# Optimization experiments

Hardware: AMD Instinct MI355X
Metric: run time of the kernel (lower is better)

Reference implementation:

```python
import jax, jax.numpy as jnp
import numpy as np
from jax import lax

HEADS = 8  # ensembles * cells

def _conv(x, w, padding, groups):
    # NCHW grouped 2D convolution, stride 1
    return lax.conv_general_dilated(
        x, w, window_strides=(1, 1), padding=padding,
        feature_group_count=groups,
        dimension_numbers=('NCHW', 'OIHW', 'NCHW'))


def setup_inputs() -> dict:
    key = jax.random.key(0)
    ks = jax.random.split(key, 16)
    N, Cin, H, W = 8, 128, 36, 36
    C = 256                      # out_channels
    hc = C // HEADS              # head_channels = 32
    s = jnp.float32(0.05)        # weight scale to keep logits sane
    f32 = jnp.float32
    inp = {
        'x':  jax.random.normal(ks[0], (N, Cin, H, W), f32),
        'h0': jnp.zeros((N, C, H, W), f32),
        'c0': jnp.zeros((N, C, H, W), f32),
        'Wx': jax.random.normal(ks[1], (C, Cin, 1, 1), f32) * s,
        'Wq': jax.random.normal(ks[2], (C, 2 * hc, 3, 3), f32) * s,
        'Wk': jax.random.normal(ks[3], (C, 2 * hc, 3, 3), f32) * s,
        'Wv': jax.random.normal(ks[4], (C, 2 * hc, 3, 3), f32) * s,
        'Wi1': jax.random.normal(ks[5], (C, hc, 1, 1), f32) * s,
        'Wi2': jax.random.normal(ks[6], (C, 2 * hc, 3, 3), f32) * s,
        'bi': jnp.zeros((C,), f32),
        'Wf1': jax.random.normal(ks[7], (C, hc, 1, 1), f32) * s,
        'Wf2': jax.random.normal(ks[8], (C, 2 * hc, 3, 3), f32) * s,
        'bf': jnp.zeros((C,), f32),
        'Wg1': jax.random.normal(ks[9], (C, hc, 1, 1), f32) * s,
        'Wg2': jax.random.normal(ks[10], (C, 2 * hc, 3, 3), f32) * s,
        'bg': jnp.zeros((C,), f32),
        'Wo1': jax.random.normal(ks[11], (C, hc, 1, 1), f32) * s,
        'Wo2': jax.random.normal(ks[12], (C, 2 * hc, 3, 3), f32) * s,
        'bo': jnp.zeros((C,), f32),
        'tau': jnp.full((HEADS,), hc ** (-0.5), f32),
    }
    return inp


def reference(x, h0, c0, Wx, Wq, Wk, Wv, Wi1, Wi2, bi,
              Wf1, Wf2, bf, Wg1, Wg2, bg, Wo1, Wo2, bo, tau):
    N, _, H, W = x.shape
    G = tau.shape[0]
    # input projection (1x1 conv, no groups, no bias)
    xx = _conv(x, Wx, 'VALID', 1)          # [N, C, H, W]
    C = xx.shape[1]
    hc = C // G
    # stack x and h per head: [N, G, 2, hc, H, W] -> [N, 2C, H, W]
    xh = jnp.stack([xx.reshape(N, G, hc, H, W),
                    h0.reshape(N, G, hc, H, W)], axis=2)
    xh = xh.reshape(N, 2 * C, H, W)
    # q padded (SAME), k/v unpadded (VALID) -> mismatched spatial extents
    q = _conv(xh, Wq, 'SAME', G).reshape(N, G, hc, H * W)          # Q = H*W
    kc = _conv(xh, Wk, 'VALID', G)
    Dh, Dw = kc.shape[2], kc.shape[3]
    k = kc.reshape(N, G, hc, Dh * Dw)                              # D = (H-ks+1)*(W-ks+1)
    v = _conv(xh, Wv, 'VALID', G).reshape(N, G, hc, Dh * Dw)
    # attention: tau-scaled channel contraction, softmax over key positions
    logits = jnp.einsum('g,ngcq,ngcd->ngqd', tau, q, k)            # [N,G,Q,D]
    attn = jax.nn.softmax(logits, axis=3)
    a = jnp.einsum('ngcd,ngqd->ngcq', v, attn).reshape(N, C, H, W)

    def gate(W1, W2, b):
        # grouped 1x1 conv on a + grouped kxk SAME conv on xh + bias
        return (_conv(a, W1, 'VALID', G) + _conv(xh, W2, 'SAME', G)
                + b[None, :, None, None])

    i = jax.nn.sigmoid(gate(Wi1, Wi2, bi))
    f = jax.nn.sigmoid(gate(Wf1, Wf2, bf))
    g = jnp.tanh(gate(Wg1, Wg2, bg))
    o = jax.nn.sigmoid(gate(Wo1, Wo2, bo))
    c = f * c0 + i * g
    h = o * jnp.tanh(c)
    return h
```

## Files before the change

### kernel.cpp

```cpp
#include <hip/hip_runtime.h>
#include <math.h>

#define NN  8
#define CIN 128
#define HW  1296
#define CC  256
#define DDS 1156

typedef __attribute__((ext_vector_type(8))) short bvec8;
typedef __attribute__((ext_vector_type(4))) float fvec4;

__device__ __forceinline__ float sigmoidf_(float x) {
    return 1.f / (1.f + __expf(-x));
}
__device__ __forceinline__ float tanhf_(float x) {
    float xa = fminf(fmaxf(x, -15.f), 15.f);
    float e = __expf(2.f * xa);
    return (e - 1.f) / (e + 1.f);
}
__device__ __forceinline__ unsigned short f2bf(float f) {
    unsigned int u = __float_as_uint(f);
    u = (u + 0x7FFFu + ((u >> 16) & 1u)) >> 16;
    return (unsigned short)u;
}
__device__ __forceinline__ unsigned int cvtpk_bf16(float a, float b) {
    unsigned int r;
    asm("v_cvt_pk_bf16_f32 %0, %1, %2" : "=v"(r) : "v"(a), "v"(b));
    return r;
}

__global__ void k_prep(const float* __restrict__ x, const float* __restrict__ h0,
                       const float* __restrict__ Wx,
                       const float* __restrict__ Wq, const float* __restrict__ Wk,
                       const float* __restrict__ Wv, const float* __restrict__ tau,
                       const float* __restrict__ Wi2, const float* __restrict__ Wf2,
                       const float* __restrict__ Wg2, const float* __restrict__ Wo2,
                       const float* __restrict__ Wi1, const float* __restrict__ Wf1,
                       const float* __restrict__ Wg1, const float* __restrict__ Wo1,
                       unsigned short* __restrict__ xb, unsigned short* __restrict__ h0b,
                       unsigned short* __restrict__ apx, unsigned short* __restrict__ apq,
                       unsigned short* __restrict__ apg2, unsigned short* __restrict__ apg1) {
    int t = blockIdx.x * 256 + threadIdx.x;
    union { unsigned short us[8]; bvec8 v; } pk;
    if (t < 165888) {
        int p = t % 1296; int t2 = t / 1296;
        int icb = t2 % 16, n = t2 / 16;
        #pragma unroll
        for (int j = 0; j < 8; ++j)
            pk.us[j] = f2bf(x[(size_t)(n * CIN + icb * 8 + j) * HW + p]);
        *(bvec8*)(xb + (size_t)t * 8) = pk.v;
    } else if (t < 497664) {
        int u = t - 165888;
        int p = u % 1296; int t2 = u / 1296;
        int ocb = t2 % 32, n = t2 / 32;
        #pragma unroll
        for (int j = 0; j < 8; ++j)
            pk.us[j] = f2bf(h0[(size_t)(n * CC + ocb * 8 + j) * HW + p]);
        *(bvec8*)(h0b + (size_t)u * 8) = pk.v;
    } else if (t < 552960) {
        int u = t - 497664;
        int lane = u & 63;
        int t2 = u >> 6;
        int mf = t2 % 6, t3 = t2 / 6;
        int s = t3 % 18, g = t3 / 18;
        int kyx = s >> 1, icb = s & 1;
        int ky = kyx / 3, kx = kyx % 3;
        int m = mf * 16 + (lane & 15);
        int conv = m >> 5, cl = m & 31, co = g * 32 + cl;
        int ic0 = icb * 32 + (lane >> 4) * 8;
        const float* W = (conv == 0) ? Wq : (conv == 1 ? Wk : Wv);
        float scale = (conv == 0) ? tau[g] : 1.f;
        #pragma unroll
        for (int j = 0; j < 8; ++j)
            pk.us[j] = f2bf(W[((co * 64 + ic0 + j) * 3 + ky) * 3 + kx] * scale);
        *(bvec8*)(apq + (size_t)u * 8) = pk.v;
    } else if (t < 557056) {
        int u = t - 552960;
        int lane = u & 63;
        int t2 = u >> 6;
        int mf = t2 % 16, s = t2 / 16;
        int co = mf * 16 + (lane & 15);
        int k0 = s * 32 + (lane >> 4) * 8;
        #pragma unroll
        for (int j = 0; j < 8; ++j)
            pk.us[j] = f2bf(Wx[co * CIN + k0 + j]);
        *(bvec8*)(apx + (size_t)u * 8) = pk.v;
    } else if (t < 630784) {
        int u = t - 557056;
        int lane = u & 63;
        int t2 = u >> 6;
        int mf = t2 % 8, t3 = t2 / 8;
        int s = t3 % 18, g = t3 / 18;
        int kyx = s >> 1, icb = s & 1;
        int ky = kyx / 3, kx = kyx % 3;
        int m = mf * 16 + (lane & 15);
        int gate = m >> 5, cl = m & 31, co = g * 32 + cl;
        int ic0 = icb * 32 + (lane >> 4) * 8;
        const float* W = (gate == 0) ? Wi2 : (gate == 1 ? Wf2 : (gate == 2 ? Wg2 : Wo2));
        #pragma unroll
        for (int j = 0; j < 8; ++j)
            pk.us[j] = f2bf(W[((co * 64 + ic0 + j) * 3 + ky) * 3 + kx]);
        *(bvec8*)(apg2 + (size_t)u * 8) = pk.v;
    } else if (t < 634880) {
        int u = t - 630784;
        int lane = u & 63;
        int t2 = u >> 6;
        int mf = t2 % 8, g = t2 / 8;
        int m = mf * 16 + (lane & 15);
        int gate = m >> 5, cl = m & 31, co = g * 32 + cl;
        int k0 = (lane >> 4) * 8;
        const float* W = (gate == 0) ? Wi1 : (gate == 1 ? Wf1 : (gate == 2 ? Wg1 : Wo1));
        #pragma unroll
        for (int j = 0; j < 8; ++j)
            pk.us[j] = f2bf(W[co * 32 + k0 + j]);
        *(bvec8*)(apg1 + (size_t)u * 8) = pk.v;
    }
}

__global__ __launch_bounds__(256) void k_xx_mfma(
        const unsigned short* __restrict__ xb, const unsigned short* __restrict__ apx,
        unsigned short* __restrict__ xxb) {
    int bid = blockIdx.x;
    int n = bid / 27, pc = bid % 27;
    int tid = threadIdx.x;
    int w = tid >> 6, lane = tid & 63;
    int ln = lane & 15, kgrp = lane >> 4;
    const bvec8* A = (const bvec8*)apx;
    bvec8 af[4][4];
    #pragma unroll
    for (int s = 0; s < 4; ++s)
        #pragma unroll
        for (int i = 0; i < 4; ++i)
            af[s][i] = A[(s * 16 + w * 4 + i) * 64 + lane];
    fvec4 acc[4][3];
    #pragma unroll
    for (int i = 0; i < 4; ++i)
        #pragma unroll
        for (int jn = 0; jn < 3; ++jn)
            acc[i][jn] = fvec4{0.f, 0.f, 0.f, 0.f};
    #pragma unroll
    for (int s = 0; s < 4; ++s) {
        #pragma unroll
        for (int jn = 0; jn < 3; ++jn) {
            int p = pc * 48 + jn * 16 + ln;
            bvec8 bfr = *(const bvec8*)(xb + ((size_t)(n * 16 + s * 4 + kgrp) * HW + p) * 8);
            #pragma unroll
            for (int i = 0; i < 4; ++i)
                acc[i][jn] = __builtin_amdgcn_mfma_f32_16x16x32_bf16(af[s][i], bfr, acc[i][jn], 0, 0, 0);
        }
    }
    #pragma unroll
    for (int i = 0; i < 4; ++i) {
        int co0 = (w * 4 + i) * 16 + kgrp * 4;
        int icb = co0 >> 3, sub = co0 & 7;
        #pragma unroll
        for (int jn = 0; jn < 3; ++jn) {
            int p = pc * 48 + jn * 16 + ln;
            union { unsigned short us[4]; unsigned long long u; } pk;
            #pragma unroll
            for (int r = 0; r < 4; ++r) pk.us[r] = f2bf(acc[i][jn][r]);
            *(unsigned long long*)(xxb + ((size_t)(n * 32 + icb) * HW + p) * 8 + sub) = pk.u;
        }
    }
}

__global__ __launch_bounds__(384) void k_qkv_mfma(
        const unsigned short* __restrict__ xxb, const unsigned short* __restrict__ h0b,
        const unsigned short* __restrict__ apq,
        unsigned short* __restrict__ qT, unsigned short* __restrict__ kT,
        unsigned short* __restrict__ vB) {
    int bid = blockIdx.x;
    int n = bid / 72, rem = bid % 72;
    int g = rem / 9, yt = rem % 9;
    __shared__ bvec8 sm[1824];
    int tid = threadIdx.x;
    for (int u = tid; u < 1824; u += 384) {
        int col = u % 38; int t2 = u / 38;
        int icb = t2 % 8; int rr = t2 / 8;
        int y = yt * 4 - 1 + rr, cx = col - 1;
        bvec8 val = {0, 0, 0, 0, 0, 0, 0, 0};
        if (y >= 0 && y < 36 && cx >= 0 && cx < 36) {
            const unsigned short* src = (icb < 4)
                ? (xxb + ((size_t)(n * 32 + g * 4 + icb) * HW) * 8)
                : (h0b + ((size_t)(n * 32 + g * 4 + icb - 4) * HW) * 8);
            val = *(const bvec8*)(src + (size_t)(y * 36 + cx) * 8);
        }
        int s = rr * 38 + col;
        sm[s * 8 + (icb ^ (s & 7))] = val;
    }
    __syncthreads();
    int lane = tid & 63, w = tid >> 6;
    int mg = w % 3, nh = w / 3;
    int kgrp = lane >> 4;
    int nf0 = nh * 4;
    int sb[5], pl[5];
    #pragma unroll
    for (int jn = 0; jn < 5; ++jn) {
        int p = (nf0 + jn) * 16 + (lane & 15);
        pl[jn] = p;
        sb[jn] = (p / 36) * 38 + (p % 36);
    }
    fvec4 acc[2][5];
    #pragma unroll
    for (int i = 0; i < 2; ++i)
        #pragma unroll
        for (int jn = 0; jn < 5; ++jn)
            acc[i][jn] = fvec4{0.f, 0.f, 0.f, 0.f};
    const bvec8* ap = (const bvec8*)apq + (size_t)g * 6912 + mg * 128 + lane;
    for (int s = 0; s < 18; ++s) {
        int kyx = s >> 1, icb = s & 1;
        int ky = kyx / 3, kx = kyx % 3;
        bvec8 a0 = ap[0], a1 = ap[64];
        ap += 384;
        int soff = ky * 38 + kx;
        int ib = icb * 4 + kgrp;
        #pragma unroll
        for (int jn = 0; jn < 5; ++jn) {
            int slot = sb[jn] + soff;
            bvec8 bfr = sm[slot * 8 + (ib ^ (slot & 7))];
            acc[0][jn] = __builtin_amdgcn_mfma_f32_16x16x32_bf16(a0, bfr, acc[0][jn], 0, 0, 0);
            acc[1][jn] = __builtin_amdgcn_mfma_f32_16x16x32_bf16(a1, bfr, acc[1][jn], 0, 0, 0);
        }
    }
    int ngb = n * 8 + g;
    unsigned short* qTg = qT + (size_t)ngb * 41472;
    unsigned short* kTg = kT + (size_t)ngb * 36992;
    unsigned short* vBg = vB + (size_t)ngb * 37120;
    #pragma unroll
    for (int i = 0; i < 2; ++i) {
        int mf = mg * 2 + i;
        int m0 = mf * 16 + kgrp * 4;
        int conv = m0 >> 5, c0 = m0 & 31;
        #pragma unroll
        for (int jn = 0; jn < 5; ++jn) {
            int gp = yt * 144 + pl[jn];
            int py = gp / 36, px = gp % 36;
            if (conv == 0) {
                union { unsigned short us[4]; unsigned long long u; } pk;
                #pragma unroll
                for (int r = 0; r < 4; ++r) pk.us[r] = f2bf(acc[i][jn][r]);
                *(unsigned long long*)(qTg + (size_t)gp * 32 + c0) = pk.u;
            } else if (py >= 1 && py <= 34 && px >= 1 && px <= 34) {
                int dpix = (py - 1) * 34 + (px - 1);
                if (conv == 1) {
                    union { unsigned short us[4]; unsigned long long u; } pk;
                    #pragma unroll
                    for (int r = 0; r < 4; ++r) pk.us[r] = f2bf(acc[i][jn][r]);
                    *(unsigned long long*)(kTg + (size_t)dpix * 32 + c0) = pk.u;
                } else {
                    #pragma unroll
                    for (int r = 0; r < 4; ++r)
                        vBg[(size_t)(c0 + r) * 1160 + dpix] = f2bf(acc[i][jn][r]);
                }
            }
        }
    }
}

__global__ __launch_bounds__(256) void k_attn_mfma(
        const unsigned short* __restrict__ qT, const unsigned short* __restrict__ kT,
        const unsigned short* __restrict__ vB, unsigned short* __restrict__ ab) {
    int bid = blockIdx.x;
    int ng = bid / 21, bt = bid % 21;
    int tid = threadIdx.x;
    int w = tid >> 6, l = tid & 63;
    int qblk = bt * 4 + w;
    bool qvalid = qblk < 81;
    int qb = qvalid ? qblk : 80;
    int ln = l & 15, g = l >> 4;
    __shared__ unsigned short sP[4][640];
    const unsigned short* qTg = qT + (size_t)ng * 41472;
    const unsigned short* kTg = kT + (size_t)ng * 36992;
    const unsigned short* vBg = vB + (size_t)ng * 37120;
    bvec8 qf = *(const bvec8*)(qTg + (size_t)(qb * 16 + ln) * 32 + g * 8);
    fvec4 acc0 = {0.f, 0.f, 0.f, 0.f}, acc1 = {0.f, 0.f, 0.f, 0.f};
    fvec4 zero = {0.f, 0.f, 0.f, 0.f};
    float lp = 0.f;
    for (int dt = 0; dt < DDS; dt += 32) {
        int d0 = dt + ln;
        bvec8 kA0 = *(const bvec8*)(kTg + (size_t)min(d0, 1155) * 32 + g * 8);
        bvec8 kA1 = *(const bvec8*)(kTg + (size_t)min(d0 + 16, 1155) * 32 + g * 8);
        bvec8 vA0 = *(const bvec8*)(vBg + (size_t)ln * 1160 + dt + g * 8);
        bvec8 vA1 = *(const bvec8*)(vBg + (size_t)(16 + ln) * 1160 + dt + g * 8);
        fvec4 s0 = __builtin_amdgcn_mfma_f32_16x16x32_bf16(kA0, qf, zero, 0, 0, 0);
        fvec4 s1 = __builtin_amdgcn_mfma_f32_16x16x32_bf16(kA1, qf, zero, 0, 0, 0);
        if (dt + 32 > DDS) {
            if (g > 0) { s0[0] = s0[1] = s0[2] = s0[3] = -1e30f; }
            s1[0] = s1[1] = s1[2] = s1[3] = -1e30f;
        }
        float p[8];
        #pragma unroll
        for (int r = 0; r < 4; ++r) {
            p[r]     = __expf(s0[r]);
            p[4 + r] = __expf(s1[r]);
        }
        lp += ((p[0] + p[1]) + (p[2] + p[3])) + ((p[4] + p[5]) + (p[6] + p[7]));
        union { unsigned int ui[2]; unsigned long long u; } w0, w1;
        w0.ui[0] = cvtpk_bf16(p[0], p[1]);
        w0.ui[1] = cvtpk_bf16(p[2], p[3]);
        w1.ui[0] = cvtpk_bf16(p[4], p[5]);
        w1.ui[1] = cvtpk_bf16(p[6], p[7]);
        *(unsigned long long*)&sP[w][ln * 40 + g * 4]      = w0.u;
        *(unsigned long long*)&sP[w][ln * 40 + 16 + g * 4] = w1.u;
        bvec8 pB = *(bvec8*)&sP[w][ln * 40 + g * 8];
        acc0 = __builtin_amdgcn_mfma_f32_16x16x32_bf16(vA0, pB, acc0, 0, 0, 0);
        acc1 = __builtin_amdgcn_mfma_f32_16x16x32_bf16(vA1, pB, acc1, 0, 0, 0);
    }
    float lt = lp;
    lt += __shfl_xor(lt, 16, 64);
    lt += __shfl_xor(lt, 32, 64);
    float inv = 1.f / lt;
    if (qvalid) {
        int qpos = qblk * 16 + ln;
        unsigned short* ag = ab + (size_t)ng * 41472;
        int sub = (g & 1) * 4;
        union { unsigned short us[4]; unsigned long long u; } pk0, pk1;
        #pragma unroll
        for (int r = 0; r < 4; ++r) {
            pk0.us[r] = f2bf(acc0[r] * inv);
            pk1.us[r] = f2bf(acc1[r] * inv);
        }
        *(unsigned long long*)(ag + ((size_t)(g >> 1) * HW + qpos) * 8 + sub)       = pk0.u;
        *(unsigned long long*)(ag + ((size_t)(2 + (g >> 1)) * HW + qpos) * 8 + sub) = pk1.u;
    }
}

__global__ __launch_bounds__(256) void k_gates_mfma(
        const unsigned short* __restrict__ xxb, const unsigned short* __restrict__ h0b,
        const float* __restrict__ c0, const unsigned short* __restrict__ ab,
        const unsigned short* __restrict__ apg2, const unsigned short* __restrict__ apg1,
        const float* __restrict__ bi, const float* __restrict__ bf_,
        const float* __restrict__ bg, const float* __restrict__ bo,
        float* __restrict__ out) {
    int bid = blockIdx.x;
    int n = bid / 72, rem = bid % 72;
    int g = rem / 9, yt = rem % 9;
    __shared__ bvec8 smx[1824];
    __shared__ bvec8 sma[576];
    int tid = threadIdx.x;
    for (int u = tid; u < 1824; u += 256) {
        int col = u % 38; int t2 = u / 38;
        int icb = t2 % 8; int rr = t2 / 8;
        int y = yt * 4 - 1 + rr, cx = col - 1;
        bvec8 val = {0, 0, 0, 0, 0, 0, 0, 0};
        if (y >= 0 && y < 36 && cx >= 0 && cx < 36) {
            const unsigned short* src = (icb < 4)
                ? (xxb + ((size_t)(n * 32 + g * 4 + icb) * HW) * 8)
                : (h0b + ((size_t)(n * 32 + g * 4 + icb - 4) * HW) * 8);
            val = *(const bvec8*)(src + (size_t)(y * 36 + cx) * 8);
        }
        int s = rr * 38 + col;
        smx[s * 8 + (icb ^ (s & 7))] = val;
    }
    int ngb = n * 8 + g;
    for (int u = tid; u < 576; u += 256) {
        int p = u % 144, cb = u / 144;
        int gp = yt * 144 + p;
        bvec8 val = *(const bvec8*)(ab + ((size_t)(ngb * 4 + cb) * HW + gp) * 8);
        sma[p * 4 + (cb ^ (p & 3))] = val;
    }
    __syncthreads();
    int lane = tid & 63, w = tid >> 6;
    int b = w & 1, nh = w >> 1;
    int kgrp = lane >> 4, nf0 = nh * 4;
    int sb[5], pl[5];
    #pragma unroll
    for (int jn = 0; jn < 5; ++jn) {
        int p = (nf0 + jn) * 16 + (lane & 15);
        pl[jn] = p;
        sb[jn] = (p / 36) * 38 + (p % 36);
    }
    fvec4 acc[4][5];
    #pragma unroll
    for (int i = 0; i < 4; ++i)
        #pragma unroll
        for (int jn = 0; jn < 5; ++jn)
            acc[i][jn] = fvec4{0.f, 0.f, 0.f, 0.f};
    const bvec8* ap = (const bvec8*)apg2 + ((size_t)g * 144 + b) * 64 + lane;
    for (int s = 0; s < 18; ++s) {
        int kyx = s >> 1, icb = s & 1;
        int ky = kyx / 3, kx = kyx % 3;
        bvec8 a0 = ap[0], a1 = ap[128], a2 = ap[256], a3 = ap[384];
        ap += 512;
        int soff = ky * 38 + kx;
        int ib = icb * 4 + kgrp;
        #pragma unroll
        for (int jn = 0; jn < 5; ++jn) {
            int slot = sb[jn] + soff;
            bvec8 bfr = smx[slot * 8 + (ib ^ (slot & 7))];
            acc[0][jn] = __builtin_amdgcn_mfma_f32_16x16x32_bf16(a0, bfr, acc[0][jn], 0, 0, 0);
            acc[1][jn] = __builtin_amdgcn_mfma_f32_16x16x32_bf16(a1, bfr, acc[1][jn], 0, 0, 0);
            acc[2][jn] = __builtin_amdgcn_mfma_f32_16x16x32_bf16(a2, bfr, acc[2][jn], 0, 0, 0);
            acc[3][jn] = __builtin_amdgcn_mfma_f32_16x16x32_bf16(a3, bfr, acc[3][jn], 0, 0, 0);
        }
    }
    {
        const bvec8* ap1 = (const bvec8*)apg1 + ((size_t)g * 8 + b) * 64 + lane;
        bvec8 a0 = ap1[0], a1 = ap1[128], a2 = ap1[256], a3 = ap1[384];
        #pragma unroll
        for (int jn = 0; jn < 5; ++jn) {
            int p = pl[jn];
            bvec8 bfr = sma[p * 4 + (kgrp ^ (p & 3))];
            acc[0][jn] = __builtin_amdgcn_mfma_f32_16x16x32_bf16(a0, bfr, acc[0][jn], 0, 0, 0);
            acc[1][jn] = __builtin_amdgcn_mfma_f32_16x16x32_bf16(a1, bfr, acc[1][jn], 0, 0, 0);
            acc[2][jn] = __builtin_amdgcn_mfma_f32_16x16x32_bf16(a2, bfr, acc[2][jn], 0, 0, 0);
            acc[3][jn] = __builtin_amdgcn_mfma_f32_16x16x32_bf16(a3, bfr, acc[3][jn], 0, 0, 0);
        }
    }
    #pragma unroll
    for (int jn = 0; jn < 5; ++jn) {
        int gp = yt * 144 + pl[jn];
        #pragma unroll
        for (int r = 0; r < 4; ++r) {
            int cl = b * 16 + kgrp * 4 + r;
            int co = g * 32 + cl;
            float ip   = acc[0][jn][r] + bi[co];
            float fp   = acc[1][jn][r] + bf_[co];
            float gpre = acc[2][jn][r] + bg[co];
            float op   = acc[3][jn][r] + bo[co];
            float iv = sigmoidf_(ip), fv = sigmoidf_(fp);
            float gv = tanhf_(gpre), ov = sigmoidf_(op);
            float cv = fmaf(fv, c0[(size_t)(n * CC + co) * HW + gp], iv * gv);
            out[(size_t)(n * CC + co) * HW + gp] = ov * tanhf_(cv);
        }
    }
}

extern "C" void kernel_launch(void* const* d_in, const int* in_sizes, int n_in,
                              void* d_out, int out_size, void* d_ws, size_t ws_size,
                              hipStream_t stream) {
    const float* x   = (const float*)d_in[0];
    const float* h0  = (const float*)d_in[1];
    const float* c0  = (const float*)d_in[2];
    const float* Wx  = (const float*)d_in[3];
    const float* Wq  = (const float*)d_in[4];
    const float* Wk  = (const float*)d_in[5];
    const float* Wv  = (const float*)d_in[6];
    const float* Wi1 = (const float*)d_in[7];
    const float* Wi2 = (const float*)d_in[8];
    const float* bi  = (const float*)d_in[9];
    const float* Wf1 = (const float*)d_in[10];
    const float* Wf2 = (const float*)d_in[11];
    const float* bf  = (const float*)d_in[12];
    const float* Wg1 = (const float*)d_in[13];
    const float* Wg2 = (const float*)d_in[14];
    const float* bg  = (const float*)d_in[15];
    const float* Wo1 = (const float*)d_in[16];
    const float* Wo2 = (const float*)d_in[17];
    const float* bo  = (const float*)d_in[18];
    const float* tau = (const float*)d_in[19];

    unsigned short* ws  = (unsigned short*)d_ws;
    unsigned short* xb   = ws;
    unsigned short* h0b  = xb   + 1327104;
    unsigned short* xxb  = h0b  + 2654208;
    unsigned short* ab   = xxb  + 2654208;
    unsigned short* qT   = ab   + 2654208;
    unsigned short* kT   = qT   + 2654208;
    unsigned short* vB   = kT   + 2367488;
    unsigned short* apx  = vB   + 2375744;
    unsigned short* apq  = apx  + 32768;
    unsigned short* apg2 = apq  + 442368;
    unsigned short* apg1 = apg2 + 589824;
    float* out = (float*)d_out;

    hipLaunchKernelGGL(k_prep, dim3(2480), dim3(256), 0, stream,
                       x, h0, Wx, Wq, Wk, Wv, tau,
                       Wi2, Wf2, Wg2, Wo2, Wi1, Wf1, Wg1, Wo1,
                       xb, h0b, apx, apq, apg2, apg1);
    hipLaunchKernelGGL(k_xx_mfma,   dim3(216),  dim3(256), 0, stream, xb, apx, xxb);
    hipLaunchKernelGGL(k_qkv_mfma,  dim3(576),  dim3(384), 0, stream, xxb, h0b, apq, qT, kT, vB);
    hipLaunchKernelGGL(k_attn_mfma, dim3(1344), dim3(256), 0, stream, qT, kT, vB, ab);
    hipLaunchKernelGGL(k_gates_mfma,dim3(576),  dim3(256), 0, stream, xxb, h0b, c0, ab,
                       apg2, apg1, bi, bf, bg, bo, out);
}
```

Baseline: 130.0 us.

## Stage input transpose through LDS, use exp2 softmax, prefetch attention K/V tiles

The prep kernel now converts x and h0 into channel-interleaved bf16 by loading 8 channel planes coalesced into shared memory and then packing them, instead of issuing strided per-thread global reads. The attention loop folds log2(e) into the tau-scaled Q weights so it can use the raw v_exp_f32 instruction. It also software-prefetches the next K/V fragments, peels the partial last tile out of the loop, and so drops the per-iteration clamp and mask. This adds LDS use in prep and more registers in the attention loop.

```diff
diff --git a/kernel.cpp b/kernel.cpp
--- a/kernel.cpp
+++ b/kernel.cpp
@@ -28,37 +28,52 @@
     asm("v_cvt_pk_bf16_f32 %0, %1, %2" : "=v"(r) : "v"(a), "v"(b));
     return r;
 }
-
-__global__ void k_prep(const float* __restrict__ x, const float* __restrict__ h0,
-                       const float* __restrict__ Wx,
-                       const float* __restrict__ Wq, const float* __restrict__ Wk,
-                       const float* __restrict__ Wv, const float* __restrict__ tau,
-                       const float* __restrict__ Wi2, const float* __restrict__ Wf2,
-                       const float* __restrict__ Wg2, const float* __restrict__ Wo2,
-                       const float* __restrict__ Wi1, const float* __restrict__ Wf1,
-                       const float* __restrict__ Wg1, const float* __restrict__ Wo1,
-                       unsigned short* __restrict__ xb, unsigned short* __restrict__ h0b,
-                       unsigned short* __restrict__ apx, unsigned short* __restrict__ apq,
-                       unsigned short* __restrict__ apg2, unsigned short* __restrict__ apg1) {
-    int t = blockIdx.x * 256 + threadIdx.x;
+__device__ __forceinline__ float exp2a(float x) {
+    float r;
+    asm("v_exp_f32 %0, %1" : "=v"(r) : "v"(x));
+    return r;
+}
+
+__global__ __launch_bounds__(256) void k_prep(
+        const float* __restrict__ x, const float* __restrict__ h0,
+        const float* __restrict__ Wx,
+        const float* __restrict__ Wq, const float* __restrict__ Wk,
+        const float* __restrict__ Wv, const float* __restrict__ tau,
+        const float* __restrict__ Wi2, const float* __restrict__ Wf2,
+        const float* __restrict__ Wg2, const float* __restrict__ Wo2,
+        const float* __restrict__ Wi1, const float* __restrict__ Wf1,
+        const float* __restrict__ Wg1, const float* __restrict__ Wo1,
+        unsigned short* __restrict__ xb, unsigned short* __restrict__ h0b,
+        unsigned short* __restrict__ apx, unsigned short* __restrict__ apq,
+        unsigned short* __restrict__ apg2, unsigned short* __restrict__ apg1) {
+    __shared__ float tr[10400];
+    int bid = blockIdx.x;
+    int tid = threadIdx.x;
+    if (bid < 384) {
+        int n = bid / 48, cb = bid % 48;
+        const float* src = (cb < 16) ? x  + (size_t)(n * CIN + cb * 8) * HW
+                                     : h0 + (size_t)(n * CC + (cb - 16) * 8) * HW;
+        unsigned short* dst = (cb < 16) ? xb  + ((size_t)(n * 16 + cb) * HW) * 8
+                                        : h0b + ((size_t)(n * 32 + (cb - 16)) * HW) * 8;
+        #pragma unroll
+        for (int c = 0; c < 8; ++c)
+            for (int p4 = tid; p4 < 324; p4 += 256) {
+                float4 v = ((const float4*)(src + (size_t)c * HW))[p4];
+                *(float4*)&tr[c * 1300 + p4 * 4] = v;
+            }
+        __syncthreads();
+        for (int p = tid; p < 1296; p += 256) {
+            union { unsigned short us[8]; bvec8 v; } pk;
+            #pragma unroll
+            for (int c = 0; c < 8; ++c) pk.us[c] = f2bf(tr[c * 1300 + p]);
+            *(bvec8*)(dst + (size_t)p * 8) = pk.v;
+        }
+        return;
+    }
+    int t = (bid - 384) * 256 + tid;
     union { unsigned short us[8]; bvec8 v; } pk;
-    if (t < 165888) {
-        int p = t % 1296; int t2 = t / 1296;
-        int icb = t2 % 16, n = t2 / 16;
-        #pragma unroll
-        for (int j = 0; j < 8; ++j)
-            pk.us[j] = f2bf(x[(size_t)(n * CIN + icb * 8 + j) * HW + p]);
-        *(bvec8*)(xb + (size_t)t * 8) = pk.v;
-    } else if (t < 497664) {
-        int u = t - 165888;
-        int p = u % 1296; int t2 = u / 1296;
-        int ocb = t2 % 32, n = t2 / 32;
-        #pragma unroll
-        for (int j = 0; j < 8; ++j)
-            pk.us[j] = f2bf(h0[(size_t)(n * CC + ocb * 8 + j) * HW + p]);
-        *(bvec8*)(h0b + (size_t)u * 8) = pk.v;
-    } else if (t < 552960) {
-        int u = t - 497664;
+    if (t < 55296) {
+        int u = t;
         int lane = u & 63;
         int t2 = u >> 6;
         int mf = t2 % 6, t3 = t2 / 6;
@@ -69,13 +84,13 @@
         int conv = m >> 5, cl = m & 31, co = g * 32 + cl;
         int ic0 = icb * 32 + (lane >> 4) * 8;
         const float* W = (conv == 0) ? Wq : (conv == 1 ? Wk : Wv);
-        float scale = (conv == 0) ? tau[g] : 1.f;
+        float scale = (conv == 0) ? tau[g] * 1.4426950408889634f : 1.f;
         #pragma unroll
         for (int j = 0; j < 8; ++j)
             pk.us[j] = f2bf(W[((co * 64 + ic0 + j) * 3 + ky) * 3 + kx] * scale);
         *(bvec8*)(apq + (size_t)u * 8) = pk.v;
-    } else if (t < 557056) {
-        int u = t - 552960;
+    } else if (t < 59392) {
+        int u = t - 55296;
         int lane = u & 63;
         int t2 = u >> 6;
         int mf = t2 % 16, s = t2 / 16;
@@ -85,8 +100,8 @@
         for (int j = 0; j < 8; ++j)
             pk.us[j] = f2bf(Wx[co * CIN + k0 + j]);
         *(bvec8*)(apx + (size_t)u * 8) = pk.v;
-    } else if (t < 630784) {
-        int u = t - 557056;
+    } else if (t < 133120) {
+        int u = t - 59392;
         int lane = u & 63;
         int t2 = u >> 6;
         int mf = t2 % 8, t3 = t2 / 8;
@@ -101,8 +116,8 @@
         for (int j = 0; j < 8; ++j)
             pk.us[j] = f2bf(W[((co * 64 + ic0 + j) * 3 + ky) * 3 + kx]);
         *(bvec8*)(apg2 + (size_t)u * 8) = pk.v;
-    } else if (t < 634880) {
-        int u = t - 630784;
+    } else if (t < 137216) {
+        int u = t - 133120;
         int lane = u & 63;
         int t2 = u >> 6;
         int mf = t2 % 8, g = t2 / 8;
@@ -273,26 +288,32 @@
     const unsigned short* kTg = kT + (size_t)ng * 36992;
     const unsigned short* vBg = vB + (size_t)ng * 37120;
     bvec8 qf = *(const bvec8*)(qTg + (size_t)(qb * 16 + ln) * 32 + g * 8);
+    const unsigned short* kp = kTg + ln * 32 + g * 8;
+    const unsigned short* vp = vBg + (size_t)ln * 1160 + g * 8;
+    unsigned short* sw0 = &sP[w][ln * 40 + g * 4];
+    unsigned short* sw1 = &sP[w][ln * 40 + 16 + g * 4];
+    const unsigned short* sr = &sP[w][ln * 40 + g * 8];
     fvec4 acc0 = {0.f, 0.f, 0.f, 0.f}, acc1 = {0.f, 0.f, 0.f, 0.f};
     fvec4 zero = {0.f, 0.f, 0.f, 0.f};
     float lp = 0.f;
-    for (int dt = 0; dt < DDS; dt += 32) {
-        int d0 = dt + ln;
-        bvec8 kA0 = *(const bvec8*)(kTg + (size_t)min(d0, 1155) * 32 + g * 8);
-        bvec8 kA1 = *(const bvec8*)(kTg + (size_t)min(d0 + 16, 1155) * 32 + g * 8);
-        bvec8 vA0 = *(const bvec8*)(vBg + (size_t)ln * 1160 + dt + g * 8);
-        bvec8 vA1 = *(const bvec8*)(vBg + (size_t)(16 + ln) * 1160 + dt + g * 8);
-        fvec4 s0 = __builtin_amdgcn_mfma_f32_16x16x32_bf16(kA0, qf, zero, 0, 0, 0);
-        fvec4 s1 = __builtin_amdgcn_mfma_f32_16x16x32_bf16(kA1, qf, zero, 0, 0, 0);
-        if (dt + 32 > DDS) {
-            if (g > 0) { s0[0] = s0[1] = s0[2] = s0[3] = -1e30f; }
-            s1[0] = s1[1] = s1[2] = s1[3] = -1e30f;
-        }
+    bvec8 ka0 = *(const bvec8*)(kp);
+    bvec8 ka1 = *(const bvec8*)(kp + 512);
+    bvec8 va0 = *(const bvec8*)(vp);
+    bvec8 va1 = *(const bvec8*)(vp + 18560);
+    #pragma unroll 2
+    for (int t = 0; t < 36; ++t) {
+        int tn = (t < 35) ? t + 1 : 35;
+        bvec8 nk0 = *(const bvec8*)(kp + tn * 1024);
+        bvec8 nk1 = *(const bvec8*)(kp + tn * 1024 + 512);
+        bvec8 nv0 = *(const bvec8*)(vp + tn * 32);
+        bvec8 nv1 = *(const bvec8*)(vp + tn * 32 + 18560);
+        fvec4 s0 = __builtin_amdgcn_mfma_f32_16x16x32_bf16(ka0, qf, zero, 0, 0, 0);
+        fvec4 s1 = __builtin_amdgcn_mfma_f32_16x16x32_bf16(ka1, qf, zero, 0, 0, 0);
         float p[8];
         #pragma unroll
         for (int r = 0; r < 4; ++r) {
-            p[r]     = __expf(s0[r]);
-            p[4 + r] = __expf(s1[r]);
+            p[r]     = exp2a(s0[r]);
+            p[4 + r] = exp2a(s1[r]);
         }
         lp += ((p[0] + p[1]) + (p[2] + p[3])) + ((p[4] + p[5]) + (p[6] + p[7]));
         union { unsigned int ui[2]; unsigned long long u; } w0, w1;
@@ -300,11 +321,31 @@
         w0.ui[1] = cvtpk_bf16(p[2], p[3]);
         w1.ui[0] = cvtpk_bf16(p[4], p[5]);
         w1.ui[1] = cvtpk_bf16(p[6], p[7]);
-        *(unsigned long long*)&sP[w][ln * 40 + g * 4]      = w0.u;
-        *(unsigned long long*)&sP[w][ln * 40 + 16 + g * 4] = w1.u;
-        bvec8 pB = *(bvec8*)&sP[w][ln * 40 + g * 8];
-        acc0 = __builtin_amdgcn_mfma_f32_16x16x32_bf16(vA0, pB, acc0, 0, 0, 0);
-        acc1 = __builtin_amdgcn_mfma_f32_16x16x32_bf16(vA1, pB, acc1, 0, 0, 0);
+        *(unsigned long long*)sw0 = w0.u;
+        *(unsigned long long*)sw1 = w1.u;
+        bvec8 pB = *(const bvec8*)sr;
+        acc0 = __builtin_amdgcn_mfma_f32_16x16x32_bf16(va0, pB, acc0, 0, 0, 0);
+        acc1 = __builtin_amdgcn_mfma_f32_16x16x32_bf16(va1, pB, acc1, 0, 0, 0);
+        ka0 = nk0; ka1 = nk1; va0 = nv0; va1 = nv1;
+    }
+    {
+        bvec8 tk = *(const bvec8*)(kTg + (size_t)min(1152 + ln, 1155) * 32 + g * 8);
+        fvec4 s0 = __builtin_amdgcn_mfma_f32_16x16x32_bf16(tk, qf, zero, 0, 0, 0);
+        float p[4];
+        #pragma unroll
+        for (int r = 0; r < 4; ++r)
+            p[r] = (g == 0) ? exp2a(s0[r]) : 0.f;
+        lp += (p[0] + p[1]) + (p[2] + p[3]);
+        union { unsigned int ui[2]; unsigned long long u; } w0;
+        w0.ui[0] = cvtpk_bf16(p[0], p[1]);
+        w0.ui[1] = cvtpk_bf16(p[2], p[3]);
+        *(unsigned long long*)sw0 = w0.u;
+        *(unsigned long long*)sw1 = 0ull;
+        bvec8 pB = *(const bvec8*)sr;
+        bvec8 tv0 = *(const bvec8*)(vp + 36 * 32);
+        bvec8 tv1 = *(const bvec8*)(vp + 36 * 32 + 18560);
+        acc0 = __builtin_amdgcn_mfma_f32_16x16x32_bf16(tv0, pB, acc0, 0, 0, 0);
+        acc1 = __builtin_amdgcn_mfma_f32_16x16x32_bf16(tv1, pB, acc1, 0, 0, 0);
     }
     float lt = lp;
     lt += __shfl_xor(lt, 16, 64);
@@ -464,7 +505,7 @@
     unsigned short* apg1 = apg2 + 589824;
     float* out = (float*)d_out;
 
-    hipLaunchKernelGGL(k_prep, dim3(2480), dim3(256), 0, stream,
+    hipLaunchKernelGGL(k_prep, dim3(920), dim3(256), 0, stream,
                        x, h0, Wx, Wq, Wk, Wv, tau,
                        Wi2, Wf2, Wg2, Wo2, Wi1, Wf1, Wg1, Wo1,
                        xb, h0b, apx, apq, apg2, apg1);
```

Result: no change. 127.4 us (-1.9%).
